# Performance work log

Hardware: AMD Instinct MI355X
Metric: run time of the kernel (lower is better)

## Reference

```python
import jax, jax.numpy as jnp
import numpy as np

SAMPLE_SIZE = 512
DOE_DIM = 10
LATENT = 32
BATCH = 8192
HID = SAMPLE_SIZE // 4   # 128
HID2 = SAMPLE_SIZE // 2  # 256


def _build_groups():
    """Replicates the encoder's per-row neighbor gather construction.
    Returns padded index table [G, Kmax] (int32) and float mask [G, Kmax]."""
    rng = np.random.RandomState(42)
    doe = rng.rand(SAMPLE_SIZE, DOE_DIM)
    sorted_doe = np.argsort(doe, axis=0)  # [S, D]
    idx_list = []
    for i in range(1, SAMPLE_SIZE - 1):
        idxs = np.unique(sorted_doe[i - 1:i + 2, :].flatten())
        idx_list.append(idxs)
    G = len(idx_list)               # sample_size - 2 = 510
    K = max(len(a) for a in idx_list)  # <= 3 * DOE_DIM
    idx = np.zeros((G, K), dtype=np.int32)
    mask = np.zeros((G, K), dtype=np.float32)
    for g, a in enumerate(idx_list):
        idx[g, :len(a)] = a
        mask[g, :len(a)] = 1.0
    return jnp.asarray(idx), jnp.asarray(mask)


def _dense_init(key, fan_in, fan_out):
    w = jax.random.normal(key, (fan_in, fan_out), dtype=jnp.float32) / jnp.sqrt(jnp.float32(fan_in))
    b = jnp.zeros((fan_out,), dtype=jnp.float32)
    return w, b


def setup_inputs() -> dict:
    key = jax.random.key(0)
    ks = jax.random.split(key, 8)
    idx, mask = _build_groups()
    G, K = idx.shape
    x = jax.random.uniform(ks[0], (BATCH, SAMPLE_SIZE), dtype=jnp.float32)
    # per-group Dense(1): weight [G, K] (padded slots zeroed by mask), bias [G]
    gw = jax.random.normal(ks[1], (G, K), dtype=jnp.float32) / jnp.sqrt(jnp.float32(K))
    gb = jnp.zeros((G,), dtype=jnp.float32)
    w1, b1 = _dense_init(ks[2], G, HID)
    w2, b2 = _dense_init(ks[3], HID, LATENT)
    dw1, db1 = _dense_init(ks[4], LATENT, HID)
    dw2, db2 = _dense_init(ks[5], HID, HID2)
    dw3, db3 = _dense_init(ks[6], HID2, SAMPLE_SIZE)
    return {"x": x, "gw": gw, "gb": gb, "w1": w1, "b1": b1, "w2": w2, "b2": b2,
            "dw1": dw1, "db1": db1, "dw2": dw2, "db2": db2, "dw3": dw3, "db3": db3,
            "idx": idx, "mask": mask}


def reference(x, gw, gb, w1, b1, w2, b2, dw1, db1, dw2, db2, dw3, db3, idx, mask):
    # Encoder: grouped gather + per-group Dense(1, relu), fused as one einsum.
    gathered = x[:, idx]                                   # [B, G, K]
    h = jax.nn.relu(jnp.einsum('bgk,gk->bg', gathered, gw * mask) + gb)  # [B, G]
    h = jax.nn.relu(h @ w1 + b1)                           # [B, ss/4]
    z = jax.nn.relu(h @ w2 + b2)                           # [B, latent]
    # Decoder MLP
    d = jax.nn.relu(z @ dw1 + db1)                         # [B, ss/4]
    d = jax.nn.relu(d @ dw2 + db2)                         # [B, ss/2]
    out = jax.nn.sigmoid(d @ dw3 + db3)                    # [B, ss]
    return out
```

## Files before the change

kernel.cpp:

```cpp
#include <hip/hip_runtime.h>
#include <hip/hip_bf16.h>

#define SAMPLE 512
#define GDIM   510
#define HID    128
#define LATENT 32
#define HID2   256
#define TB     16
#define NT     512

typedef unsigned short u16;
typedef unsigned int   u32;
typedef __attribute__((ext_vector_type(8))) short s16x8;
typedef __attribute__((ext_vector_type(4))) float f32x4;

#define WGP_OFF   0
#define W1P_OFF   (WGP_OFF  + 32*16*512)
#define W2P_OFF   (W1P_OFF  + 8*16*512)
#define DW1P_OFF  (W2P_OFF  + 2*4*512)
#define DW2P_OFF  (DW1P_OFF + 8*1*512)
#define DW3P_OFF  (DW2P_OFF + 16*4*512)
#define PACK_U16  (DW3P_OFF + 32*8*512)
#define NCHUNK    (PACK_U16 / 8)

__device__ __forceinline__ u16 f2b(float f) {
    union { float f; u32 i; } v; v.f = f;
    return (u16)((v.i + 0x7FFFu + ((v.i >> 16) & 1u)) >> 16);
}

__global__ __launch_bounds__(256) void pack_all(
    const float* __restrict__ w1, const float* __restrict__ w2,
    const float* __restrict__ dw1, const float* __restrict__ dw2,
    const float* __restrict__ dw3, u16* __restrict__ ws)
{
    int c = blockIdx.x * 256 + threadIdx.x;
    if (c >= NCHUNK) return;
    if (c < W1P_OFF / 8) {
        *(s16x8*)(ws + (size_t)c * 8) = (s16x8)0;
        return;
    }
    const float* W; int Kd, Nd, KT, base;
    if      (c < W2P_OFF / 8)  { W = w1;  Kd = GDIM;   Nd = HID;    KT = 16; base = W1P_OFF / 8; }
    else if (c < DW1P_OFF / 8) { W = w2;  Kd = HID;    Nd = LATENT; KT = 4;  base = W2P_OFF / 8; }
    else if (c < DW2P_OFF / 8) { W = dw1; Kd = LATENT; Nd = HID;    KT = 1;  base = DW1P_OFF / 8; }
    else if (c < DW3P_OFF / 8) { W = dw2; Kd = HID;    Nd = HID2;   KT = 4;  base = DW2P_OFF / 8; }
    else                       { W = dw3; Kd = HID2;   Nd = SAMPLE; KT = 8;  base = DW3P_OFF / 8; }
    int c2   = c - base;
    int lane = c2 & 63;
    int kt   = (c2 >> 6) % KT;
    int nt   = (c2 >> 6) / KT;
    int n    = nt * 16 + (lane & 15);
    int k0   = kt * 32 + (lane >> 4) * 8;
    u16 tmp[8];
    #pragma unroll
    for (int j = 0; j < 8; ++j) {
        int k = k0 + j;
        float v = (k < Kd && n < Nd) ? W[(size_t)k * Nd + n] : 0.f;
        tmp[j] = f2b(v);
    }
    *(s16x8*)(ws + (size_t)c * 8) = *(s16x8*)tmp;
}

__global__ __launch_bounds__(256) void scatter_gw(
    const float* __restrict__ gw, const float* __restrict__ mask,
    const int* __restrict__ idx, u16* __restrict__ ws, int total, int K)
{
    int t = blockIdx.x * 256 + threadIdx.x;
    if (t >= total) return;
    float m = mask[t];
    if (m == 0.f) return;
    int g = t / K;
    int s = idx[t];
    float v = gw[t] * m;
    int nt = g >> 4, kt = s >> 5;
    int lane = ((s >> 3) & 3) * 16 + (g & 15);
    int j = s & 7;
    ws[WGP_OFF + (size_t)(((nt * 16 + kt) * 64 + lane) * 8 + j)] = f2b(v);
}

template<int KT, int NTN, int TPW>
__device__ __forceinline__ void mfma_phase(
    int wave, int lane,
    const u16* inl, int sin,
    const u16* __restrict__ pW,
    const float* bias,
    u16* outl, int sout)
{
    if (NTN < 8 && wave >= NTN) return;
    const u16* arow = inl + (lane & 15) * sin + (lane >> 4) * 8;
    f32x4 acc[TPW];
    #pragma unroll
    for (int i = 0; i < TPW; ++i) acc[i] = (f32x4){0.f, 0.f, 0.f, 0.f};
    #pragma unroll
    for (int kt = 0; kt < KT; ++kt) {
        s16x8 a = *(const s16x8*)(arow + kt * 32);
        #pragma unroll
        for (int i = 0; i < TPW; ++i) {
            int nt = wave + 8 * i;
            s16x8 b = *(const s16x8*)(pW + (size_t)((nt * KT + kt) * 64 + lane) * 8);
            acc[i] = __builtin_amdgcn_mfma_f32_16x16x32_bf16(a, b, acc[i], 0, 0, 0);
        }
    }
    #pragma unroll
    for (int i = 0; i < TPW; ++i) {
        int nt = wave + 8 * i;
        int col = nt * 16 + (lane & 15);
        float bs = bias[col];
        #pragma unroll
        for (int r = 0; r < 4; ++r) {
            int row = (lane >> 4) * 4 + r;
            float v = acc[i][r] + bs;
            outl[row * sout + col] = f2b(v > 0.f ? v : 0.f);
        }
    }
}

__global__ __launch_bounds__(NT) void ae_mfma(
    const float* __restrict__ x,
    const float* __restrict__ gb,  const float* __restrict__ b1,
    const float* __restrict__ b2,  const float* __restrict__ db1,
    const float* __restrict__ db2, const float* __restrict__ db3,
    const u16*   __restrict__ ws,
    float* __restrict__ out)
{
    __shared__ __align__(16) u16 xs[TB * 520];
    __shared__ __align__(16) u16 h1[TB * 520];
    __shared__ __align__(16) u16 h2[TB * 136];
    __shared__ __align__(16) u16 zz[TB * 40];
    __shared__ __align__(16) u16 d1[TB * 136];
    __shared__ __align__(16) u16 d2[TB * 264];
    __shared__ float biases[1568];

    const int tid  = threadIdx.x;
    const int wave = tid >> 6;
    const int lane = tid & 63;
    const int b0   = blockIdx.x * TB;

    biases[tid]        = (tid < GDIM) ? gb[tid] : 0.f;
    biases[1056 + tid] = db3[tid];
    if (tid < 128) biases[512 + tid] = b1[tid];
    if (tid < 32)  biases[640 + tid] = b2[tid];
    if (tid < 128) biases[672 + tid] = db1[tid];
    if (tid < 256) biases[800 + tid] = db2[tid];

    {
        const float4* xg = (const float4*)(x + (size_t)b0 * SAMPLE);
        #pragma unroll
        for (int it = 0; it < (TB * SAMPLE / 4) / NT; ++it) {
            int v = it * NT + tid;
            float4 f = xg[v];
            int row = v >> 7;
            int cp  = (v & 127) * 4;
            u16* p = xs + row * 520 + cp;
            u16 t4[4] = { f2b(f.x), f2b(f.y), f2b(f.z), f2b(f.w) };
            *(unsigned long long*)p = *(unsigned long long*)t4;
        }
    }
    __syncthreads();

    mfma_phase<16, 32, 4>(wave, lane, xs, 520, ws + WGP_OFF,  biases,       h1, 520);
    __syncthreads();
    mfma_phase<16, 8, 1>(wave, lane, h1, 520, ws + W1P_OFF,  biases + 512, h2, 136);
    __syncthreads();
    mfma_phase<4, 2, 1>(wave, lane, h2, 136, ws + W2P_OFF,  biases + 640, zz, 40);
    __syncthreads();
    mfma_phase<1, 8, 1>(wave, lane, zz, 40,  ws + DW1P_OFF, biases + 672, d1, 136);
    __syncthreads();
    mfma_phase<4, 16, 2>(wave, lane, d1, 136, ws + DW2P_OFF, biases + 800, d2, 264);
    __syncthreads();

    {
        const u16* arow = d2 + (lane & 15) * 264 + (lane >> 4) * 8;
        const u16* pW = ws + DW3P_OFF;
        f32x4 acc[4];
        #pragma unroll
        for (int i = 0; i < 4; ++i) acc[i] = (f32x4){0.f, 0.f, 0.f, 0.f};
        #pragma unroll
        for (int kt = 0; kt < 8; ++kt) {
            s16x8 a = *(const s16x8*)(arow + kt * 32);
            #pragma unroll
            for (int i = 0; i < 4; ++i) {
                int nt = wave + 8 * i;
                s16x8 b = *(const s16x8*)(pW + (size_t)((nt * 8 + kt) * 64 + lane) * 8);
                acc[i] = __builtin_amdgcn_mfma_f32_16x16x32_bf16(a, b, acc[i], 0, 0, 0);
            }
        }
        #pragma unroll
        for (int i = 0; i < 4; ++i) {
            int nt = wave + 8 * i;
            int col = nt * 16 + (lane & 15);
            float bs = biases[1056 + col];
            #pragma unroll
            for (int r = 0; r < 4; ++r) {
                int row = (lane >> 4) * 4 + r;
                float v = acc[i][r] + bs;
                out[(size_t)(b0 + row) * SAMPLE + col] = 1.f / (1.f + __expf(-v));
            }
        }
    }
}

extern "C" void kernel_launch(void* const* d_in, const int* in_sizes, int n_in,
                              void* d_out, int out_size, void* d_ws, size_t ws_size,
                              hipStream_t stream) {
    const float* x   = (const float*)d_in[0];
    const float* gw  = (const float*)d_in[1];
    const float* gb  = (const float*)d_in[2];
    const float* w1  = (const float*)d_in[3];
    const float* b1  = (const float*)d_in[4];
    const float* w2  = (const float*)d_in[5];
    const float* b2  = (const float*)d_in[6];
    const float* dw1 = (const float*)d_in[7];
    const float* db1 = (const float*)d_in[8];
    const float* dw2 = (const float*)d_in[9];
    const float* db2 = (const float*)d_in[10];
    const float* dw3 = (const float*)d_in[11];
    const float* db3 = (const float*)d_in[12];
    const int* idx   = (const int*)d_in[13];
    const float* mask= (const float*)d_in[14];
    float* out = (float*)d_out;
    u16* ws = (u16*)d_ws;

    const int B  = in_sizes[0] / SAMPLE;
    const int G  = in_sizes[2];
    const int K  = in_sizes[1] / G;
    const int GK = in_sizes[1];

    pack_all<<<(NCHUNK + 255) / 256, 256, 0, stream>>>(w1, w2, dw1, dw2, dw3, ws);
    scatter_gw<<<(GK + 255) / 256, 256, 0, stream>>>(gw, mask, idx, ws, GK, K);
    ae_mfma<<<B / TB, NT, 0, stream>>>(x, gb, b1, b2, db1, db2, db3, ws, out);
}
```

Measured before the change: 123.2 us.

## Process two row tiles per block to reuse weight fragments and alias LDS buffers

Doubles the batch rows per block from 16 to 32, so each weight fragment loaded from global memory feeds two MFMAs (one per 16-row tile), halving weight traffic per row. Shared-memory buffers are merged into one aliased arena so that dead stages' space is reused and the larger tile still fits, and launch bounds request four blocks per CU. The cost is doubled accumulator registers and half as many blocks (256), which may reduce occupancy and tail balance on a large-CU GPU.

After: 119.6 us. -2.9%, faster.

```diff
diff --git a/kernel.cpp b/kernel.cpp
--- a/kernel.cpp
+++ b/kernel.cpp
@@ -6,7 +6,7 @@
 #define HID    128
 #define LATENT 32
 #define HID2   256
-#define TB     16
+#define TB     32
 #define NT     512
 
 typedef unsigned short u16;
@@ -87,18 +87,24 @@
     u16* outl, int sout)
 {
     if (NTN < 8 && wave >= NTN) return;
-    const u16* arow = inl + (lane & 15) * sin + (lane >> 4) * 8;
-    f32x4 acc[TPW];
-    #pragma unroll
-    for (int i = 0; i < TPW; ++i) acc[i] = (f32x4){0.f, 0.f, 0.f, 0.f};
+    const u16* arow0 = inl + (lane & 15) * sin + (lane >> 4) * 8;
+    const u16* arow1 = arow0 + 16 * sin;
+    f32x4 acc[TPW][2];
+    #pragma unroll
+    for (int i = 0; i < TPW; ++i) {
+        acc[i][0] = (f32x4){0.f, 0.f, 0.f, 0.f};
+        acc[i][1] = (f32x4){0.f, 0.f, 0.f, 0.f};
+    }
     #pragma unroll
     for (int kt = 0; kt < KT; ++kt) {
-        s16x8 a = *(const s16x8*)(arow + kt * 32);
+        s16x8 a0 = *(const s16x8*)(arow0 + kt * 32);
+        s16x8 a1 = *(const s16x8*)(arow1 + kt * 32);
         #pragma unroll
         for (int i = 0; i < TPW; ++i) {
             int nt = wave + 8 * i;
             s16x8 b = *(const s16x8*)(pW + (size_t)((nt * KT + kt) * 64 + lane) * 8);
-            acc[i] = __builtin_amdgcn_mfma_f32_16x16x32_bf16(a, b, acc[i], 0, 0, 0);
+            acc[i][0] = __builtin_amdgcn_mfma_f32_16x16x32_bf16(a0, b, acc[i][0], 0, 0, 0);
+            acc[i][1] = __builtin_amdgcn_mfma_f32_16x16x32_bf16(a1, b, acc[i][1], 0, 0, 0);
         }
     }
     #pragma unroll
@@ -107,15 +113,26 @@
         int col = nt * 16 + (lane & 15);
         float bs = bias[col];
         #pragma unroll
-        for (int r = 0; r < 4; ++r) {
-            int row = (lane >> 4) * 4 + r;
-            float v = acc[i][r] + bs;
-            outl[row * sout + col] = f2b(v > 0.f ? v : 0.f);
-        }
-    }
-}
-
-__global__ __launch_bounds__(NT) void ae_mfma(
+        for (int mt = 0; mt < 2; ++mt) {
+            #pragma unroll
+            for (int r = 0; r < 4; ++r) {
+                int row = mt * 16 + (lane >> 4) * 4 + r;
+                float v = acc[i][mt][r] + bs;
+                outl[row * sout + col] = f2b(v > 0.f ? v : 0.f);
+            }
+        }
+    }
+}
+
+#define XS_OFF 0
+#define H2_OFF 0
+#define ZZ_OFF 4352
+#define D1_OFF 5632
+#define D2_OFF 9984
+#define H1_OFF 18432
+#define SMEM_U16 35072
+
+__global__ __launch_bounds__(NT, 4) void ae_mfma(
     const float* __restrict__ x,
     const float* __restrict__ gb,  const float* __restrict__ b1,
     const float* __restrict__ b2,  const float* __restrict__ db1,
@@ -123,13 +140,14 @@
     const u16*   __restrict__ ws,
     float* __restrict__ out)
 {
-    __shared__ __align__(16) u16 xs[TB * 520];
-    __shared__ __align__(16) u16 h1[TB * 520];
-    __shared__ __align__(16) u16 h2[TB * 136];
-    __shared__ __align__(16) u16 zz[TB * 40];
-    __shared__ __align__(16) u16 d1[TB * 136];
-    __shared__ __align__(16) u16 d2[TB * 264];
+    __shared__ __align__(16) u16 smem[SMEM_U16];
     __shared__ float biases[1568];
+    u16* xs = smem + XS_OFF;
+    u16* h1 = smem + H1_OFF;
+    u16* h2 = smem + H2_OFF;
+    u16* zz = smem + ZZ_OFF;
+    u16* d1 = smem + D1_OFF;
+    u16* d2 = smem + D2_OFF;
 
     const int tid  = threadIdx.x;
     const int wave = tid >> 6;
@@ -170,19 +188,25 @@
     __syncthreads();
 
     {
-        const u16* arow = d2 + (lane & 15) * 264 + (lane >> 4) * 8;
+        const u16* arow0 = d2 + (lane & 15) * 264 + (lane >> 4) * 8;
+        const u16* arow1 = arow0 + 16 * 264;
         const u16* pW = ws + DW3P_OFF;
-        f32x4 acc[4];
-        #pragma unroll
-        for (int i = 0; i < 4; ++i) acc[i] = (f32x4){0.f, 0.f, 0.f, 0.f};
+        f32x4 acc[4][2];
+        #pragma unroll
+        for (int i = 0; i < 4; ++i) {
+            acc[i][0] = (f32x4){0.f, 0.f, 0.f, 0.f};
+            acc[i][1] = (f32x4){0.f, 0.f, 0.f, 0.f};
+        }
         #pragma unroll
         for (int kt = 0; kt < 8; ++kt) {
-            s16x8 a = *(const s16x8*)(arow + kt * 32);
+            s16x8 a0 = *(const s16x8*)(arow0 + kt * 32);
+            s16x8 a1 = *(const s16x8*)(arow1 + kt * 32);
             #pragma unroll
             for (int i = 0; i < 4; ++i) {
                 int nt = wave + 8 * i;
                 s16x8 b = *(const s16x8*)(pW + (size_t)((nt * 8 + kt) * 64 + lane) * 8);
-                acc[i] = __builtin_amdgcn_mfma_f32_16x16x32_bf16(a, b, acc[i], 0, 0, 0);
+                acc[i][0] = __builtin_amdgcn_mfma_f32_16x16x32_bf16(a0, b, acc[i][0], 0, 0, 0);
+                acc[i][1] = __builtin_amdgcn_mfma_f32_16x16x32_bf16(a1, b, acc[i][1], 0, 0, 0);
             }
         }
         #pragma unroll
@@ -191,10 +215,13 @@
             int col = nt * 16 + (lane & 15);
             float bs = biases[1056 + col];
             #pragma unroll
-            for (int r = 0; r < 4; ++r) {
-                int row = (lane >> 4) * 4 + r;
-                float v = acc[i][r] + bs;
-                out[(size_t)(b0 + row) * SAMPLE + col] = 1.f / (1.f + __expf(-v));
+            for (int mt = 0; mt < 2; ++mt) {
+                #pragma unroll
+                for (int r = 0; r < 4; ++r) {
+                    int row = mt * 16 + (lane >> 4) * 4 + r;
+                    float v = acc[i][mt][r] + bs;
+                    out[(size_t)(b0 + row) * SAMPLE + col] = 1.f / (1.f + __expf(-v));
+                }
             }
         }
     }
```

## Split fused autoencoder into per-layer tiled GEMM kernels with LDS-staged weights

Applied to the files above, without the earlier changes.

Replaces the single fused kernel, which streamed packed weights from global memory for each 16-row batch tile, with six separate per-layer GEMM launches. Each launch stages a weight slice and a 64-row activation tile into LDS, and intermediate activations go through global workspace as bf16. The x-to-bf16 conversion and the gather-weight scatter are folded into the packing kernel, which builds the group weights per output chunk instead of scattering them. The aim is more weight reuse per block and better occupancy. The cost is extra launches and round trips of intermediates through global memory.

Result: slower. 153.6 us (+24.7%).

```diff
diff --git a/kernel.cpp b/kernel.cpp
--- a/kernel.cpp
+++ b/kernel.cpp
@@ -6,8 +6,7 @@
 #define HID    128
 #define LATENT 32
 #define HID2   256
-#define TB     16
-#define NT     512
+#define BATCH  8192
 
 typedef unsigned short u16;
 typedef unsigned int   u32;
@@ -23,20 +22,60 @@
 #define PACK_U16  (DW3P_OFF + 32*8*512)
 #define NCHUNK    (PACK_U16 / 8)
 
+#define XB_OFF  524288
+#define H1_OFF  (XB_OFF + BATCH*SAMPLE)
+#define H2_OFF  (H1_OFF + BATCH*SAMPLE)
+#define ZZ_OFF  (H2_OFF + BATCH*HID)
+#define D1_OFF  (ZZ_OFF + BATCH*LATENT)
+#define D2_OFF  (D1_OFF + BATCH*HID)
+
+#define XCONV   (BATCH*SAMPLE/8)
+
 __device__ __forceinline__ u16 f2b(float f) {
     union { float f; u32 i; } v; v.f = f;
     return (u16)((v.i + 0x7FFFu + ((v.i >> 16) & 1u)) >> 16);
 }
 
 __global__ __launch_bounds__(256) void pack_all(
+    const float* __restrict__ x,
     const float* __restrict__ w1, const float* __restrict__ w2,
     const float* __restrict__ dw1, const float* __restrict__ dw2,
-    const float* __restrict__ dw3, u16* __restrict__ ws)
+    const float* __restrict__ dw3,
+    const float* __restrict__ gw, const float* __restrict__ mask,
+    const int* __restrict__ idx,
+    u16* __restrict__ ws, int G, int K)
 {
     int c = blockIdx.x * 256 + threadIdx.x;
-    if (c >= NCHUNK) return;
+    if (c >= NCHUNK + XCONV) return;
+    u16 tmp[8];
+    if (c >= NCHUNK) {
+        int cx = c - NCHUNK;
+        const float4* xp = (const float4*)(x + (size_t)cx * 8);
+        float4 f0 = xp[0], f1 = xp[1];
+        tmp[0]=f2b(f0.x); tmp[1]=f2b(f0.y); tmp[2]=f2b(f0.z); tmp[3]=f2b(f0.w);
+        tmp[4]=f2b(f1.x); tmp[5]=f2b(f1.y); tmp[6]=f2b(f1.z); tmp[7]=f2b(f1.w);
+        *(s16x8*)(ws + XB_OFF + (size_t)cx * 8) = *(s16x8*)tmp;
+        return;
+    }
     if (c < W1P_OFF / 8) {
-        *(s16x8*)(ws + (size_t)c * 8) = (s16x8)0;
+        int lane = c & 63;
+        int kt   = (c >> 6) & 15;
+        int nt   = (c >> 6) >> 4;
+        int g    = nt * 16 + (lane & 15);
+        int k0   = kt * 32 + (lane >> 4) * 8;
+        #pragma unroll
+        for (int j = 0; j < 8; ++j) tmp[j] = 0;
+        if (g < G) {
+            const int*   idxr = idx  + (size_t)g * K;
+            const float* gwr  = gw   + (size_t)g * K;
+            const float* mr   = mask + (size_t)g * K;
+            for (int t = 0; t < K; ++t) {
+                int j = idxr[t] - k0;
+                float m = mr[t];
+                if ((unsigned)j < 8u && m > 0.f) tmp[j] = f2b(gwr[t] * m);
+            }
+        }
+        *(s16x8*)(ws + (size_t)c * 8) = *(s16x8*)tmp;
         return;
     }
     const float* W; int Kd, Nd, KT, base;
@@ -51,7 +90,6 @@
     int nt   = (c2 >> 6) / KT;
     int n    = nt * 16 + (lane & 15);
     int k0   = kt * 32 + (lane >> 4) * 8;
-    u16 tmp[8];
     #pragma unroll
     for (int j = 0; j < 8; ++j) {
         int k = k0 + j;
@@ -61,140 +99,72 @@
     *(s16x8*)(ws + (size_t)c * 8) = *(s16x8*)tmp;
 }
 
-__global__ __launch_bounds__(256) void scatter_gw(
-    const float* __restrict__ gw, const float* __restrict__ mask,
-    const int* __restrict__ idx, u16* __restrict__ ws, int total, int K)
+template<int KT, int NS16, int OUT_SIG>
+__global__ __launch_bounds__(512) void gemm_phase(
+    const u16* __restrict__ ws_ro, u16* __restrict__ ws_wr,
+    const float* __restrict__ bias, int bias_n,
+    float* __restrict__ fout,
+    int in_off, int w_off, int out_off, int n_total, int nsl)
 {
-    int t = blockIdx.x * 256 + threadIdx.x;
-    if (t >= total) return;
-    float m = mask[t];
-    if (m == 0.f) return;
-    int g = t / K;
-    int s = idx[t];
-    float v = gw[t] * m;
-    int nt = g >> 4, kt = s >> 5;
-    int lane = ((s >> 3) & 3) * 16 + (g & 15);
-    int j = s & 7;
-    ws[WGP_OFF + (size_t)(((nt * 16 + kt) * 64 + lane) * 8 + j)] = f2b(v);
-}
-
-template<int KT, int NTN, int TPW>
-__device__ __forceinline__ void mfma_phase(
-    int wave, int lane,
-    const u16* inl, int sin,
-    const u16* __restrict__ pW,
-    const float* bias,
-    u16* outl, int sout)
-{
-    if (NTN < 8 && wave >= NTN) return;
-    const u16* arow = inl + (lane & 15) * sin + (lane >> 4) * 8;
-    f32x4 acc[TPW];
-    #pragma unroll
-    for (int i = 0; i < TPW; ++i) acc[i] = (f32x4){0.f, 0.f, 0.f, 0.f};
+    constexpr int KTOT  = KT * 32;
+    constexpr int SIN   = KTOT + 8;
+    constexpr int TBR   = 64;
+    constexpr int WSPAN = NS16 * KT * 512;
+    constexpr int NPW   = NS16 / 2;
+    __shared__ __align__(16) u16 wt[WSPAN];
+    __shared__ __align__(16) u16 xt[TBR * SIN];
+
+    const int tid  = threadIdx.x;
+    const int wave = tid >> 6;
+    const int lane = tid & 63;
+    const int rt   = blockIdx.x / nsl;
+    const int ns   = blockIdx.x % nsl;
+
+    {
+        const u16* src = ws_ro + w_off + (size_t)ns * WSPAN;
+        for (int off = tid * 8; off < WSPAN; off += 512 * 8)
+            *(s16x8*)(wt + off) = *(const s16x8*)(src + off);
+    }
+    {
+        const u16* src = ws_ro + in_off + (size_t)rt * TBR * KTOT;
+        for (int off = tid * 8; off < TBR * KTOT; off += 512 * 8) {
+            int row = off / KTOT;
+            int col = off - row * KTOT;
+            *(s16x8*)(xt + row * SIN + col) = *(const s16x8*)(src + off);
+        }
+    }
+    __syncthreads();
+
+    const int m   = wave & 3;
+    const int ng0 = (wave >> 2) * NPW;
+    const u16* arow = xt + (m * 16 + (lane & 15)) * SIN + (lane >> 4) * 8;
+    f32x4 acc[NPW];
+    #pragma unroll
+    for (int i = 0; i < NPW; ++i) acc[i] = (f32x4){0.f, 0.f, 0.f, 0.f};
     #pragma unroll
     for (int kt = 0; kt < KT; ++kt) {
         s16x8 a = *(const s16x8*)(arow + kt * 32);
         #pragma unroll
-        for (int i = 0; i < TPW; ++i) {
-            int nt = wave + 8 * i;
-            s16x8 b = *(const s16x8*)(pW + (size_t)((nt * KT + kt) * 64 + lane) * 8);
+        for (int i = 0; i < NPW; ++i) {
+            int nt = ng0 + i;
+            s16x8 b = *(const s16x8*)(wt + ((nt * KT + kt) * 64 + lane) * 8);
             acc[i] = __builtin_amdgcn_mfma_f32_16x16x32_bf16(a, b, acc[i], 0, 0, 0);
         }
     }
     #pragma unroll
-    for (int i = 0; i < TPW; ++i) {
-        int nt = wave + 8 * i;
-        int col = nt * 16 + (lane & 15);
-        float bs = bias[col];
+    for (int i = 0; i < NPW; ++i) {
+        int nt   = ng0 + i;
+        int colg = ns * (NS16 * 16) + nt * 16 + (lane & 15);
+        float bs = (colg < bias_n) ? bias[colg] : 0.f;
         #pragma unroll
         for (int r = 0; r < 4; ++r) {
-            int row = (lane >> 4) * 4 + r;
+            int rowg = rt * TBR + m * 16 + (lane >> 4) * 4 + r;
             float v = acc[i][r] + bs;
-            outl[row * sout + col] = f2b(v > 0.f ? v : 0.f);
-        }
-    }
-}
-
-__global__ __launch_bounds__(NT) void ae_mfma(
-    const float* __restrict__ x,
-    const float* __restrict__ gb,  const float* __restrict__ b1,
-    const float* __restrict__ b2,  const float* __restrict__ db1,
-    const float* __restrict__ db2, const float* __restrict__ db3,
-    const u16*   __restrict__ ws,
-    float* __restrict__ out)
-{
-    __shared__ __align__(16) u16 xs[TB * 520];
-    __shared__ __align__(16) u16 h1[TB * 520];
-    __shared__ __align__(16) u16 h2[TB * 136];
-    __shared__ __align__(16) u16 zz[TB * 40];
-    __shared__ __align__(16) u16 d1[TB * 136];
-    __shared__ __align__(16) u16 d2[TB * 264];
-    __shared__ float biases[1568];
-
-    const int tid  = threadIdx.x;
-    const int wave = tid >> 6;
-    const int lane = tid & 63;
-    const int b0   = blockIdx.x * TB;
-
-    biases[tid]        = (tid < GDIM) ? gb[tid] : 0.f;
-    biases[1056 + tid] = db3[tid];
-    if (tid < 128) biases[512 + tid] = b1[tid];
-    if (tid < 32)  biases[640 + tid] = b2[tid];
-    if (tid < 128) biases[672 + tid] = db1[tid];
-    if (tid < 256) biases[800 + tid] = db2[tid];
-
-    {
-        const float4* xg = (const float4*)(x + (size_t)b0 * SAMPLE);
-        #pragma unroll
-        for (int it = 0; it < (TB * SAMPLE / 4) / NT; ++it) {
-            int v = it * NT + tid;
-            float4 f = xg[v];
-            int row = v >> 7;
-            int cp  = (v & 127) * 4;
-            u16* p = xs + row * 520 + cp;
-            u16 t4[4] = { f2b(f.x), f2b(f.y), f2b(f.z), f2b(f.w) };
-            *(unsigned long long*)p = *(unsigned long long*)t4;
-        }
-    }
-    __syncthreads();
-
-    mfma_phase<16, 32, 4>(wave, lane, xs, 520, ws + WGP_OFF,  biases,       h1, 520);
-    __syncthreads();
-    mfma_phase<16, 8, 1>(wave, lane, h1, 520, ws + W1P_OFF,  biases + 512, h2, 136);
-    __syncthreads();
-    mfma_phase<4, 2, 1>(wave, lane, h2, 136, ws + W2P_OFF,  biases + 640, zz, 40);
-    __syncthreads();
-    mfma_phase<1, 8, 1>(wave, lane, zz, 40,  ws + DW1P_OFF, biases + 672, d1, 136);
-    __syncthreads();
-    mfma_phase<4, 16, 2>(wave, lane, d1, 136, ws + DW2P_OFF, biases + 800, d2, 264);
-    __syncthreads();
-
-    {
-        const u16* arow = d2 + (lane & 15) * 264 + (lane >> 4) * 8;
-        const u16* pW = ws + DW3P_OFF;
-        f32x4 acc[4];
-        #pragma unroll
-        for (int i = 0; i < 4; ++i) acc[i] = (f32x4){0.f, 0.f, 0.f, 0.f};
-        #pragma unroll
-        for (int kt = 0; kt < 8; ++kt) {
-            s16x8 a = *(const s16x8*)(arow + kt * 32);
-            #pragma unroll
-            for (int i = 0; i < 4; ++i) {
-                int nt = wave + 8 * i;
-                s16x8 b = *(const s16x8*)(pW + (size_t)((nt * 8 + kt) * 64 + lane) * 8);
-                acc[i] = __builtin_amdgcn_mfma_f32_16x16x32_bf16(a, b, acc[i], 0, 0, 0);
-            }
-        }
-        #pragma unroll
-        for (int i = 0; i < 4; ++i) {
-            int nt = wave + 8 * i;
-            int col = nt * 16 + (lane & 15);
-            float bs = biases[1056 + col];
-            #pragma unroll
-            for (int r = 0; r < 4; ++r) {
-                int row = (lane >> 4) * 4 + r;
-                float v = acc[i][r] + bs;
-                out[(size_t)(b0 + row) * SAMPLE + col] = 1.f / (1.f + __expf(-v));
+            if (OUT_SIG) {
+                fout[(size_t)rowg * n_total + colg] = 1.f / (1.f + __expf(-v));
+            } else {
+                v = v > 0.f ? v : 0.f;
+                ws_wr[out_off + (size_t)rowg * n_total + colg] = f2b(v);
             }
         }
     }
@@ -221,12 +191,22 @@
     float* out = (float*)d_out;
     u16* ws = (u16*)d_ws;
 
-    const int B  = in_sizes[0] / SAMPLE;
-    const int G  = in_sizes[2];
-    const int K  = in_sizes[1] / G;
-    const int GK = in_sizes[1];
-
-    pack_all<<<(NCHUNK + 255) / 256, 256, 0, stream>>>(w1, w2, dw1, dw2, dw3, ws);
-    scatter_gw<<<(GK + 255) / 256, 256, 0, stream>>>(gw, mask, idx, ws, GK, K);
-    ae_mfma<<<B / TB, NT, 0, stream>>>(x, gb, b1, b2, db1, db2, db3, ws, out);
-}
+    const int G = in_sizes[2];
+    const int K = in_sizes[1] / G;
+
+    pack_all<<<(NCHUNK + XCONV + 255) / 256, 256, 0, stream>>>(
+        x, w1, w2, dw1, dw2, dw3, gw, mask, idx, ws, G, K);
+
+    gemm_phase<16, 4, 0><<<1024, 512, 0, stream>>>(
+        ws, ws, gb, GDIM, out, XB_OFF, WGP_OFF, H1_OFF, SAMPLE, 8);
+    gemm_phase<16, 4, 0><<<256, 512, 0, stream>>>(
+        ws, ws, b1, HID, out, H1_OFF, W1P_OFF, H2_OFF, HID, 2);
+    gemm_phase<4, 2, 0><<<128, 512, 0, stream>>>(
+        ws, ws, b2, LATENT, out, H2_OFF, W2P_OFF, ZZ_OFF, LATENT, 1);
+    gemm_phase<1, 8, 0><<<128, 512, 0, stream>>>(
+        ws, ws, db1, HID, out, ZZ_OFF, DW1P_OFF, D1_OFF, HID, 1);
+    gemm_phase<4, 8, 0><<<256, 512, 0, stream>>>(
+        ws, ws, db2, HID2, out, D1_OFF, DW2P_OFF, D2_OFF, HID2, 2);
+    gemm_phase<8, 4, 1><<<1024, 512, 0, stream>>>(
+        ws, ws, db3, SAMPLE, out, D2_OFF, DW3P_OFF, 0, SAMPLE, 8);
+}
```

## Merge weight packing and gw scatter into one kernel, alias LDS buffers

Applied to the files above, without the earlier changes.

Replaces the separate pack_all and scatter_gw launches with one build_ws kernel. In it, each thread building a gather-weight chunk scans its group's idx/gw/mask row and fills the bf16 chunk directly, so the zero-fill-then-scatter ordering is no longer needed. The kernel also runs a 'warm' pass that reads all weight tensors into cache before packing, using a dummy guarded store to keep the loads alive. In the main kernel, the shared buffers are aliased into one smaller LDS region and launch_bounds asks for 4 blocks per CU, aiming at higher occupancy, at some risk of register pressure.

Result: no change. 125.4 us (+1.8%).

```diff
diff --git a/kernel.cpp b/kernel.cpp
--- a/kernel.cpp
+++ b/kernel.cpp
@@ -22,21 +22,78 @@
 #define DW3P_OFF  (DW2P_OFF + 16*4*512)
 #define PACK_U16  (DW3P_OFF + 32*8*512)
 #define NCHUNK    (PACK_U16 / 8)
+#define BW_NTH    (512 * 256)
 
 __device__ __forceinline__ u16 f2b(float f) {
     union { float f; u32 i; } v; v.f = f;
     return (u16)((v.i + 0x7FFFu + ((v.i >> 16) & 1u)) >> 16);
 }
 
-__global__ __launch_bounds__(256) void pack_all(
+__global__ __launch_bounds__(256) void build_ws(
     const float* __restrict__ w1, const float* __restrict__ w2,
     const float* __restrict__ dw1, const float* __restrict__ dw2,
-    const float* __restrict__ dw3, u16* __restrict__ ws)
+    const float* __restrict__ dw3,
+    const float* __restrict__ gw, const float* __restrict__ mask,
+    const int* __restrict__ idx,
+    u16* __restrict__ ws, int G, int K)
 {
-    int c = blockIdx.x * 256 + threadIdx.x;
+    int t = blockIdx.x * 256 + threadIdx.x;
+
+    float wa = 0.f;
+    {
+        const int gk4 = (G * K) / 4;
+        if (t < gk4) {
+            float4 a = ((const float4*)gw)[t];
+            float4 b = ((const float4*)mask)[t];
+            float4 c = ((const float4*)idx)[t];
+            wa += a.x + b.x + c.x;
+        }
+        #define WARM(P, NF) { int n4 = (NF) / 4; \
+            for (int i = t; i < n4; i += BW_NTH) { float4 a = ((const float4*)(P))[i]; wa += a.x + a.w; } }
+        WARM(w1,  GDIM * HID)
+        WARM(w2,  HID * LATENT)
+        WARM(dw1, LATENT * HID)
+        WARM(dw2, HID * HID2)
+        WARM(dw3, HID2 * SAMPLE)
+        #undef WARM
+        if (wa == 123456789.0f) ws[PACK_U16 + (t & 1023)] = 1;
+    }
+
+    int c = t;
     if (c >= NCHUNK) return;
+    u16 tmp[8];
     if (c < W1P_OFF / 8) {
-        *(s16x8*)(ws + (size_t)c * 8) = (s16x8)0;
+        int lane = c & 63;
+        int kt   = (c >> 6) & 15;
+        int nt   = (c >> 6) >> 4;
+        int g    = nt * 16 + (lane & 15);
+        int k0   = kt * 32 + (lane >> 4) * 8;
+        #pragma unroll
+        for (int j = 0; j < 8; ++j) tmp[j] = 0;
+        if (g < G) {
+            const int*   idxr = idx  + (size_t)g * K;
+            const float* gwr  = gw   + (size_t)g * K;
+            const float* mr   = mask + (size_t)g * K;
+            int tt = 0;
+            for (; tt + 4 <= K; tt += 4) {
+                int   j0 = idxr[tt]     - k0, j1 = idxr[tt + 1] - k0;
+                int   j2 = idxr[tt + 2] - k0, j3 = idxr[tt + 3] - k0;
+                float m0 = mr[tt],     m1 = mr[tt + 1];
+                float m2 = mr[tt + 2], m3 = mr[tt + 3];
+                float v0 = gwr[tt],     v1 = gwr[tt + 1];
+                float v2 = gwr[tt + 2], v3 = gwr[tt + 3];
+                if ((unsigned)j0 < 8u && m0 > 0.f) tmp[j0] = f2b(v0 * m0);
+                if ((unsigned)j1 < 8u && m1 > 0.f) tmp[j1] = f2b(v1 * m1);
+                if ((unsigned)j2 < 8u && m2 > 0.f) tmp[j2] = f2b(v2 * m2);
+                if ((unsigned)j3 < 8u && m3 > 0.f) tmp[j3] = f2b(v3 * m3);
+            }
+            for (; tt < K; ++tt) {
+                int j = idxr[tt] - k0;
+                float m = mr[tt];
+                if ((unsigned)j < 8u && m > 0.f) tmp[j] = f2b(gwr[tt] * m);
+            }
+        }
+        *(s16x8*)(ws + (size_t)c * 8) = *(s16x8*)tmp;
         return;
     }
     const float* W; int Kd, Nd, KT, base;
@@ -51,7 +108,6 @@
     int nt   = (c2 >> 6) / KT;
     int n    = nt * 16 + (lane & 15);
     int k0   = kt * 32 + (lane >> 4) * 8;
-    u16 tmp[8];
     #pragma unroll
     for (int j = 0; j < 8; ++j) {
         int k = k0 + j;
@@ -59,23 +115,6 @@
         tmp[j] = f2b(v);
     }
     *(s16x8*)(ws + (size_t)c * 8) = *(s16x8*)tmp;
-}
-
-__global__ __launch_bounds__(256) void scatter_gw(
-    const float* __restrict__ gw, const float* __restrict__ mask,
-    const int* __restrict__ idx, u16* __restrict__ ws, int total, int K)
-{
-    int t = blockIdx.x * 256 + threadIdx.x;
-    if (t >= total) return;
-    float m = mask[t];
-    if (m == 0.f) return;
-    int g = t / K;
-    int s = idx[t];
-    float v = gw[t] * m;
-    int nt = g >> 4, kt = s >> 5;
-    int lane = ((s >> 3) & 3) * 16 + (g & 15);
-    int j = s & 7;
-    ws[WGP_OFF + (size_t)(((nt * 16 + kt) * 64 + lane) * 8 + j)] = f2b(v);
 }
 
 template<int KT, int NTN, int TPW>
@@ -115,7 +154,15 @@
     }
 }
 
-__global__ __launch_bounds__(NT) void ae_mfma(
+#define XS_OFF 0
+#define H2_OFF 0
+#define ZZ_OFF 2176
+#define D1_OFF 2816
+#define D2_OFF 5120
+#define H1_OFF 9216
+#define SMEM_U16 17536
+
+__global__ __launch_bounds__(NT, 4) void ae_mfma(
     const float* __restrict__ x,
     const float* __restrict__ gb,  const float* __restrict__ b1,
     const float* __restrict__ b2,  const float* __restrict__ db1,
@@ -123,13 +170,14 @@
     const u16*   __restrict__ ws,
     float* __restrict__ out)
 {
-    __shared__ __align__(16) u16 xs[TB * 520];
-    __shared__ __align__(16) u16 h1[TB * 520];
-    __shared__ __align__(16) u16 h2[TB * 136];
-    __shared__ __align__(16) u16 zz[TB * 40];
-    __shared__ __align__(16) u16 d1[TB * 136];
-    __shared__ __align__(16) u16 d2[TB * 264];
+    __shared__ __align__(16) u16 smem[SMEM_U16];
     __shared__ float biases[1568];
+    u16* xs = smem + XS_OFF;
+    u16* h1 = smem + H1_OFF;
+    u16* h2 = smem + H2_OFF;
+    u16* zz = smem + ZZ_OFF;
+    u16* d1 = smem + D1_OFF;
+    u16* d2 = smem + D2_OFF;
 
     const int tid  = threadIdx.x;
     const int wave = tid >> 6;
@@ -224,9 +272,8 @@
     const int B  = in_sizes[0] / SAMPLE;
     const int G  = in_sizes[2];
     const int K  = in_sizes[1] / G;
-    const int GK = in_sizes[1];
-
-    pack_all<<<(NCHUNK + 255) / 256, 256, 0, stream>>>(w1, w2, dw1, dw2, dw3, ws);
-    scatter_gw<<<(GK + 255) / 256, 256, 0, stream>>>(gw, mask, idx, ws, GK, K);
+
+    build_ws<<<512, 256, 0, stream>>>(w1, w2, dw1, dw2, dw3,
+                                      gw, mask, idx, ws, G, K);
     ae_mfma<<<B / TB, NT, 0, stream>>>(x, gb, b1, b2, db1, db2, db3, ws, out);
 }
```
